# Optimization experiments

Measured on AMD Instinct MI355X. Metric: run time of the kernel, lower is better.

The kernel has to match this reference:

```python
import jax, jax.numpy as jnp
import numpy as np

NUM_HEADS = 16
GROUP_NUM = 4
HIDDEN = 1024
HEAD_DIM = HIDDEN // NUM_HEADS
EPS = 1e-5


def layernorm(x, g, b):
    mu = jnp.mean(x, axis=-1, keepdims=True)
    var = jnp.var(x, axis=-1, keepdims=True)
    return (x - mu) * jax.lax.rsqrt(var + EPS) * g + b


def setup_inputs() -> dict:
    key = jax.random.key(0)
    ks = jax.random.split(key, 12)
    s = 0.02
    return {
        "hidden_state": jax.random.normal(ks[0], (2, 2048, HIDDEN), jnp.float32),
        "wq": jax.random.normal(ks[1], (HIDDEN, HIDDEN), jnp.float32) * s,
        "bq": jnp.zeros((HIDDEN,), jnp.float32),
        "wk": jax.random.normal(ks[2], (GROUP_NUM * HEAD_DIM, HIDDEN), jnp.float32) * s,
        "bk": jnp.zeros((GROUP_NUM * HEAD_DIM,), jnp.float32),
        "wv": jax.random.normal(ks[3], (GROUP_NUM * HEAD_DIM, HIDDEN), jnp.float32) * s,
        "bv": jnp.zeros((GROUP_NUM * HEAD_DIM,), jnp.float32),
        "wo": jax.random.normal(ks[4], (HIDDEN, HIDDEN), jnp.float32) * s,
        "bo": jnp.zeros((HIDDEN,), jnp.float32),
        "ln_g": jnp.ones((HIDDEN,), jnp.float32),
        "ln_b": jnp.zeros((HIDDEN,), jnp.float32),
        "w1": jax.random.normal(ks[5], (HIDDEN, HIDDEN), jnp.float32) * s,
        "b1": jnp.zeros((HIDDEN,), jnp.float32),
        "w2": jax.random.normal(ks[6], (HIDDEN, HIDDEN), jnp.float32) * s,
        "b2": jnp.zeros((HIDDEN,), jnp.float32),
        "fln_g": jnp.ones((HIDDEN,), jnp.float32),
        "fln_b": jnp.zeros((HIDDEN,), jnp.float32),
    }


def reference(hidden_state, wq, bq, wk, bk, wv, bv, wo, bo, ln_g, ln_b,
              w1, b1, w2, b2, fln_g, fln_b):
    B, S, H = hidden_state.shape
    hpg = NUM_HEADS // GROUP_NUM  # heads per KV group

    q = hidden_state @ wq.T + bq  # [B,S,H]
    k = hidden_state @ wk.T + bk  # [B,S,G*D]
    v = hidden_state @ wv.T + bv

    q = q.reshape(B, S, NUM_HEADS, HEAD_DIM).transpose(0, 2, 1, 3)      # [B,Hh,S,D]
    k = k.reshape(B, S, GROUP_NUM, HEAD_DIM).transpose(0, 2, 1, 3)      # [B,G,S,D]
    v = v.reshape(B, S, GROUP_NUM, HEAD_DIM).transpose(0, 2, 1, 3)
    # expand KV groups to full head count (consecutive repeat, matching torch expand+reshape)
    k = jnp.repeat(k, hpg, axis=1)  # [B,Hh,S,D]
    v = jnp.repeat(v, hpg, axis=1)

    scale = 1.0 / jnp.sqrt(jnp.float32(HEAD_DIM))
    scores = jnp.einsum('bhsd,bhtd->bhst', q, k) * scale  # [B,Hh,S,S]
    probs = jax.nn.softmax(scores, axis=-1)
    attn = jnp.einsum('bhst,bhtd->bhsd', probs, v)  # [B,Hh,S,D]

    # Faithful to source: transpose(-1,-2) then raw flat view to [B, S, Hh*D]
    attn = jnp.swapaxes(attn, -1, -2).reshape(B, -1, HEAD_DIM * NUM_HEADS)

    out = layernorm(hidden_state + attn @ wo.T + bo, ln_g, ln_b)
    ffn = out @ w1.T + b1
    ffn = jax.nn.relu(ffn) @ w2.T + b2
    return layernorm(out + ffn, fln_g, fln_b)
```

## Files before the change

kernel.cpp:

```cpp
#include <hip/hip_runtime.h>
#include <math.h>

#define HIDDEN 1024
#define SEQ 2048

typedef __attribute__((ext_vector_type(8))) short short8;
typedef __attribute__((ext_vector_type(4))) float f32x4;

__device__ __forceinline__ unsigned short f2bf(float x) {
  union { float f; unsigned u; } c; c.f = x;
  unsigned r = c.u + 0x7FFFu + ((c.u >> 16) & 1u);
  return (unsigned short)(r >> 16);
}
__device__ __forceinline__ float bf2f(unsigned short h) {
  union { unsigned u; float f; } c; c.u = ((unsigned)h) << 16;
  return c.f;
}

__device__ __forceinline__ float fexp2(float x) {
  float r; asm("v_exp_f32 %0, %1" : "=v"(r) : "v"(x)); return r;
}

__device__ __forceinline__ unsigned cvt_pk_bf16(float lo, float hi) {
  unsigned r;
  asm("v_cvt_pk_bf16_f32 %0, %1, %2" : "=v"(r) : "v"(lo), "v"(hi));
  return r;
}

__device__ __forceinline__ void async_copy16(const void* g, void* l) {
  __builtin_amdgcn_global_load_lds(
      (const __attribute__((address_space(1))) unsigned int*)g,
      (__attribute__((address_space(3))) unsigned int*)l, 16, 0, 0);
}

__global__ __launch_bounds__(256) void cvt_all(
    const float* __restrict__ hs, const float* __restrict__ wq,
    const float* __restrict__ wk, const float* __restrict__ wv,
    const float* __restrict__ wo, const float* __restrict__ w1,
    const float* __restrict__ w2,
    unsigned short* __restrict__ hsb, unsigned short* __restrict__ wqb,
    unsigned short* __restrict__ wkb, unsigned short* __restrict__ wvb,
    unsigned short* __restrict__ wob, unsigned short* __restrict__ w1b,
    unsigned short* __restrict__ w2b)
{
  const int i = blockIdx.x * 256 + threadIdx.x;
  const float* src; unsigned short* dst; int off;
  if (i < 1048576)      { src = hs; dst = hsb; off = i; }
  else if (i < 1310720) { src = wq; dst = wqb; off = i - 1048576; }
  else if (i < 1376256) { src = wk; dst = wkb; off = i - 1310720; }
  else if (i < 1441792) { src = wv; dst = wvb; off = i - 1376256; }
  else if (i < 1703936) { src = wo; dst = wob; off = i - 1441792; }
  else if (i < 1966080) { src = w1; dst = w1b; off = i - 1703936; }
  else                  { src = w2; dst = w2b; off = i - 1966080; }
  float4 v = ((const float4*)src)[off];
  ushort4 o;
  o.x = f2bf(v.x); o.y = f2bf(v.y); o.z = f2bf(v.z); o.w = f2bf(v.w);
  ((ushort4*)dst)[off] = o;
}

template<bool RELU>
__global__ __launch_bounds__(256, 3) void gemm_wn(
    const unsigned short* __restrict__ A, const unsigned short* __restrict__ W,
    const float* __restrict__ bias, unsigned short* __restrict__ C,
    int M, int N, int K)
{
  __shared__ unsigned short As[2][64 * 64];
  __shared__ unsigned short Bs[2][128 * 64];

  const int flat = blockIdx.x;
  const int swz = (flat & 7) * ((int)gridDim.x >> 3) + (flat >> 3);
  const int ntx = N >> 7;
  const int m0 = (swz / ntx) * 64, n0 = (swz % ntx) * 128;

  const int tid = threadIdx.x;
  const int lane = tid & 63, wave = tid >> 6;
  const int ln = lane & 15, quad = lane >> 4;
  const int wm = (wave >> 1) * 32, wn = (wave & 1) * 64;

  f32x4 acc[2][4];
#pragma unroll
  for (int i = 0; i < 2; ++i)
#pragma unroll
    for (int j = 0; j < 4; ++j) acc[i][j] = (f32x4){0.f, 0.f, 0.f, 0.f};

  for (int k0 = 0; k0 < K; k0 += 128) {
#pragma unroll
    for (int half = 0; half < 2; ++half) {
      const int kh = k0 + half * 64;
#pragma unroll
      for (int it = 0; it < 2; ++it) {
        const int c = (wave * 2 + it) * 64 + lane;
        const int row = c >> 3, gc = (c & 7) ^ (row & 7);
        async_copy16(A + (size_t)(m0 + row) * K + kh + gc * 8,
                     &As[half][(wave * 2 + it) * 512]);
      }
#pragma unroll
      for (int it = 0; it < 4; ++it) {
        const int c = (wave * 4 + it) * 64 + lane;
        const int row = c >> 3, gc = (c & 7) ^ (row & 7);
        async_copy16(W + (size_t)(n0 + row) * K + kh + gc * 8,
                     &Bs[half][(wave * 4 + it) * 512]);
      }
    }
    __syncthreads();

#pragma unroll
    for (int half = 0; half < 2; ++half) {
      short8 af[2][2], bfr[4][2];
#pragma unroll
      for (int i = 0; i < 2; ++i) {
        const int row = wm + i * 16 + ln;
#pragma unroll
        for (int f = 0; f < 2; ++f) {
          const int ch = row * 8 + ((f * 4 + quad) ^ (row & 7));
          af[i][f] = *(const short8*)&As[half][ch * 8];
        }
      }
#pragma unroll
      for (int j = 0; j < 4; ++j) {
        const int row = wn + j * 16 + ln;
#pragma unroll
        for (int f = 0; f < 2; ++f) {
          const int ch = row * 8 + ((f * 4 + quad) ^ (row & 7));
          bfr[j][f] = *(const short8*)&Bs[half][ch * 8];
        }
      }
#pragma unroll
      for (int i = 0; i < 2; ++i)
#pragma unroll
        for (int j = 0; j < 4; ++j) {
          acc[i][j] = __builtin_amdgcn_mfma_f32_16x16x32_bf16(af[i][0], bfr[j][0], acc[i][j], 0, 0, 0);
          acc[i][j] = __builtin_amdgcn_mfma_f32_16x16x32_bf16(af[i][1], bfr[j][1], acc[i][j], 0, 0, 0);
        }
    }
    __syncthreads();
  }

#pragma unroll
  for (int j = 0; j < 4; ++j) {
    const int n = n0 + wn + j * 16 + ln;
    const float bv = bias[n];
#pragma unroll
    for (int i = 0; i < 2; ++i) {
#pragma unroll
      for (int rr = 0; rr < 4; ++rr) {
        const int m = m0 + wm + i * 16 + quad * 4 + rr;
        float v = acc[i][j][rr] + bv;
        if (RELU) v = fmaxf(v, 0.f);
        C[(size_t)m * N + n] = f2bf(v);
      }
    }
  }
}

__global__ __launch_bounds__(256) void gemm_qkv(
    const unsigned short* __restrict__ A,
    const unsigned short* __restrict__ Wq, const unsigned short* __restrict__ Wk,
    const unsigned short* __restrict__ Wv,
    const float* __restrict__ bq, const float* __restrict__ bk,
    const float* __restrict__ bv,
    unsigned short* __restrict__ Qo, unsigned short* __restrict__ Ko,
    unsigned short* __restrict__ Vt)
{
  __shared__ unsigned short As[64 * 64];
  __shared__ unsigned short Bs[128 * 64];

  const int flat = blockIdx.x;
  const int swz = (flat & 7) * 96 + (flat >> 3);
  const int bx = swz % 12, by = swz / 12;

  int mode, nw0;
  const unsigned short* W;
  const float* bias;
  if (bx < 8)       { mode = 0; W = Wq; bias = bq; nw0 = bx * 128; }
  else if (bx < 10) { mode = 1; W = Wk; bias = bk; nw0 = (bx - 8) * 128; }
  else              { mode = 2; W = Wv; bias = bv; nw0 = (bx - 10) * 128; }

  const int tid = threadIdx.x;
  const int lane = tid & 63, wave = tid >> 6;
  const int ln = lane & 15, quad = lane >> 4;
  const int wm = (wave >> 1) * 32, wn = (wave & 1) * 64;
  const int m0 = by * 64;
  const int K = 1024;

  f32x4 acc[2][4];
#pragma unroll
  for (int i = 0; i < 2; ++i)
#pragma unroll
    for (int j = 0; j < 4; ++j) acc[i][j] = (f32x4){0.f, 0.f, 0.f, 0.f};

  for (int k0 = 0; k0 < K; k0 += 64) {
#pragma unroll
    for (int it = 0; it < 2; ++it) {
      const int c = (wave * 2 + it) * 64 + lane;
      const int row = c >> 3, gc = (c & 7) ^ (row & 7);
      async_copy16(A + (size_t)(m0 + row) * K + k0 + gc * 8,
                   &As[(wave * 2 + it) * 512]);
    }
#pragma unroll
    for (int it = 0; it < 4; ++it) {
      const int c = (wave * 4 + it) * 64 + lane;
      const int row = c >> 3, gc = (c & 7) ^ (row & 7);
      async_copy16(W + (size_t)(nw0 + row) * K + k0 + gc * 8,
                   &Bs[(wave * 4 + it) * 512]);
    }
    __syncthreads();

    short8 af[2][2], bfr[4][2];
#pragma unroll
    for (int i = 0; i < 2; ++i) {
      const int row = wm + i * 16 + ln;
#pragma unroll
      for (int f = 0; f < 2; ++f) {
        const int ch = row * 8 + ((f * 4 + quad) ^ (row & 7));
        af[i][f] = *(const short8*)&As[ch * 8];
      }
    }
#pragma unroll
    for (int j = 0; j < 4; ++j) {
      const int row = wn + j * 16 + ln;
#pragma unroll
      for (int f = 0; f < 2; ++f) {
        const int ch = row * 8 + ((f * 4 + quad) ^ (row & 7));
        bfr[j][f] = *(const short8*)&Bs[ch * 8];
      }
    }
#pragma unroll
    for (int i = 0; i < 2; ++i)
#pragma unroll
      for (int j = 0; j < 4; ++j) {
        acc[i][j] = __builtin_amdgcn_mfma_f32_16x16x32_bf16(af[i][0], bfr[j][0], acc[i][j], 0, 0, 0);
        acc[i][j] = __builtin_amdgcn_mfma_f32_16x16x32_bf16(af[i][1], bfr[j][1], acc[i][j], 0, 0, 0);
      }
    __syncthreads();
  }

#pragma unroll
  for (int j = 0; j < 4; ++j) {
    const int nl = nw0 + wn + j * 16 + ln;
    const float bvv = bias[nl];
#pragma unroll
    for (int i = 0; i < 2; ++i) {
#pragma unroll
      for (int rr = 0; rr < 4; ++rr) {
        const int m = m0 + wm + i * 16 + quad * 4 + rr;
        const float v = acc[i][j][rr] + bvv;
        if (mode == 0) {
          Qo[(size_t)m * 1024 + nl] = f2bf(v);
        } else if (mode == 1) {
          Ko[(size_t)m * 256 + nl] = f2bf(v);
        } else {
          const int b = m >> 11, s = m & 2047;
          Vt[((size_t)b * 256 + nl) * SEQ + s] = f2bf(v);
        }
      }
    }
  }
}

__global__ __launch_bounds__(256, 2) void attn_mfma(
    const unsigned short* __restrict__ Q, const unsigned short* __restrict__ Kb,
    const unsigned short* __restrict__ Vt,
    unsigned short* __restrict__ N0, unsigned short* __restrict__ N1,
    float* __restrict__ LS)
{
  __shared__ unsigned short Ks[2][64 * 64];
  __shared__ unsigned short Vs[2][64 * 64];

  const int hwb = blockIdx.x;
  const int swz = (hwb & 7) * 64 + (hwb >> 3);
  const int qblk = swz & 7, half = (swz >> 3) & 1, h = (swz >> 4) & 15, b = swz >> 8;
  const int g = h >> 2;

  unsigned short* __restrict__ numO = half ? N1 : N0;
  float* __restrict__ lsO = LS + half * 65536;

  const int tid = threadIdx.x, lane = tid & 63, wave = tid >> 6;
  const int ln = lane & 15, quad = lane >> 4, q8 = quad * 8;
  const int s0 = qblk * 256;
  const float qscale = 0.125f * 1.44269504f;

  const int ln7 = ln & 7;
  const int x0 = (quad ^ ln7) * 8;
  const int x1 = ((4 + quad) ^ ln7) * 8;

  short8 ones;
#pragma unroll
  for (int e = 0; e < 8; ++e) ones[e] = (short)0x3F80;

  short8 qf[4][2];
#pragma unroll
  for (int qg = 0; qg < 4; ++qg) {
    const unsigned short* qsrc =
        Q + ((size_t)(b * SEQ + s0 + wave * 64 + qg * 16 + ln)) * 1024 + h * 64 + q8;
    qf[qg][0] = *(const short8*)qsrc;
    qf[qg][1] = *(const short8*)(qsrc + 32);
#pragma unroll
    for (int e = 0; e < 8; ++e) {
      qf[qg][0][e] = (short)f2bf(bf2f((unsigned short)qf[qg][0][e]) * qscale);
      qf[qg][1][e] = (short)f2bf(bf2f((unsigned short)qf[qg][1][e]) * qscale);
    }
  }

  const int srow = lane >> 3;
  const int sgcc = (lane & 7) ^ srow;

  auto stage = [&](int t0, int p) {
#pragma unroll
    for (int it = 0; it < 2; ++it) {
      const int row = wave * 16 + it * 8 + srow;
      const int skey = (row & 32) | ((row & 8) << 1) | ((row & 4) << 1) |
                       ((row & 16) >> 2) | (row & 3);
      async_copy16(Kb + (size_t)(b * SEQ + t0 + skey) * 256 + g * 64 + sgcc * 8,
                   &Ks[p][(wave * 2 + it) * 512]);
      async_copy16(Vt + (size_t)(b * 256 + g * 64 + row) * SEQ + t0 + sgcc * 8,
                   &Vs[p][(wave * 2 + it) * 512]);
    }
  };

  f32x4 of[4][4];
  f32x4 ls[4];
#pragma unroll
  for (int qg = 0; qg < 4; ++qg) {
    ls[qg] = (f32x4){0.f, 0.f, 0.f, 0.f};
#pragma unroll
    for (int jd = 0; jd < 4; ++jd) of[qg][jd] = (f32x4){0.f, 0.f, 0.f, 0.f};
  }

  const int tbase = half * 16;
  stage(tbase * 64, 0);

  for (int tt = 0; tt < 16; ++tt) {
    const int p = tt & 1;
    if (tt < 15) {
      stage((tbase + tt + 1) * 64, p ^ 1);
      asm volatile("s_waitcnt vmcnt(4)" ::: "memory");
    } else {
      asm volatile("s_waitcnt vmcnt(0)" ::: "memory");
    }
    __builtin_amdgcn_s_barrier();
    asm volatile("" ::: "memory");

    short8 pf[4][2];
#pragma unroll
    for (int hf = 0; hf < 2; ++hf) {
      f32x4 sc[2][4];
#pragma unroll
      for (int jn = 0; jn < 4; ++jn) {
        const int krow = (jn * 16 + ln) * 64;
        const short8 kf0 = *(const short8*)&Ks[p][krow + x0];
        const short8 kf1 = *(const short8*)&Ks[p][krow + x1];
#pragma unroll
        for (int q2 = 0; q2 < 2; ++q2) {
          const int qg = hf * 2 + q2;
          f32x4 z = (f32x4){0.f, 0.f, 0.f, 0.f};
          z = __builtin_amdgcn_mfma_f32_16x16x32_bf16(kf0, qf[qg][0], z, 0, 0, 0);
          z = __builtin_amdgcn_mfma_f32_16x16x32_bf16(kf1, qf[qg][1], z, 0, 0, 0);
          sc[q2][jn] = z;
        }
      }
#pragma unroll
      for (int q2 = 0; q2 < 2; ++q2) {
        const int qg = hf * 2 + q2;
#pragma unroll
        for (int jn = 0; jn < 4; ++jn)
#pragma unroll
          for (int r = 0; r < 4; ++r) sc[q2][jn][r] = fexp2(sc[q2][jn][r]);
#pragma unroll
        for (int F = 0; F < 2; ++F) {
          union { unsigned u[4]; short8 s; } pk;
          pk.u[0] = cvt_pk_bf16(sc[q2][2 * F][0], sc[q2][2 * F][1]);
          pk.u[1] = cvt_pk_bf16(sc[q2][2 * F][2], sc[q2][2 * F][3]);
          pk.u[2] = cvt_pk_bf16(sc[q2][2 * F + 1][0], sc[q2][2 * F + 1][1]);
          pk.u[3] = cvt_pk_bf16(sc[q2][2 * F + 1][2], sc[q2][2 * F + 1][3]);
          pf[qg][F] = pk.s;
        }
        ls[qg] = __builtin_amdgcn_mfma_f32_16x16x32_bf16(pf[qg][0], ones, ls[qg], 0, 0, 0);
        ls[qg] = __builtin_amdgcn_mfma_f32_16x16x32_bf16(pf[qg][1], ones, ls[qg], 0, 0, 0);
      }
    }

#pragma unroll
    for (int jd = 0; jd < 4; ++jd) {
      const int vrow = (jd * 16 + ln) * 64;
      const short8 vf0 = *(const short8*)&Vs[p][vrow + x0];
      const short8 vf1 = *(const short8*)&Vs[p][vrow + x1];
#pragma unroll
      for (int qg = 0; qg < 4; ++qg) {
        of[qg][jd] = __builtin_amdgcn_mfma_f32_16x16x32_bf16(pf[qg][0], vf0, of[qg][jd], 0, 0, 0);
        of[qg][jd] = __builtin_amdgcn_mfma_f32_16x16x32_bf16(pf[qg][1], vf1, of[qg][jd], 0, 0, 0);
      }
    }

    asm volatile("" ::: "memory");
    __builtin_amdgcn_s_barrier();
    asm volatile("" ::: "memory");
  }

#pragma unroll
  for (int qg = 0; qg < 4; ++qg) {
    const int sbase = s0 + wave * 64 + qg * 16 + quad * 4;
    if (ln == 0) {
#pragma unroll
      for (int r = 0; r < 4; ++r)
        lsO[(b * 16 + h) * 2048 + sbase + r] = ls[qg][r];
    }
#pragma unroll
    for (int jd = 0; jd < 4; ++jd) {
      const int d = jd * 16 + ln;
      ushort4 ov;
      ov.x = f2bf(of[qg][jd][0]);
      ov.y = f2bf(of[qg][jd][1]);
      ov.z = f2bf(of[qg][jd][2]);
      ov.w = f2bf(of[qg][jd][3]);
      *(ushort4*)&numO[((size_t)b * 1024 + h * 64 + d) * SEQ + sbase] = ov;
    }
  }
}

__global__ __launch_bounds__(256) void attn_reduce(
    const unsigned short* __restrict__ N0, unsigned short* att,
    const float* __restrict__ LS)
{
  const int i = (blockIdx.x * 256 + threadIdx.x) * 4;
  const int row = i >> 11, s = i & 2047;
  const int h = (row >> 6) & 15, b = row >> 10;
  const int lsi = (b * 16 + h) * 2048 + s;
  const float4 l0 = *(const float4*)&LS[lsi];
  const float4 l1 = *(const float4*)&LS[65536 + lsi];
  const ushort4 a = *(const ushort4*)&N0[i];
  const ushort4 c = *(const ushort4*)&att[i];
  ushort4 o;
  o.x = f2bf((bf2f(a.x) + bf2f(c.x)) / (l0.x + l1.x));
  o.y = f2bf((bf2f(a.y) + bf2f(c.y)) / (l0.y + l1.y));
  o.z = f2bf((bf2f(a.z) + bf2f(c.z)) / (l0.z + l1.z));
  o.w = f2bf((bf2f(a.w) + bf2f(c.w)) / (l0.w + l1.w));
  *(ushort4*)&att[i] = o;
}

__device__ __forceinline__ void ln_core(float x[4], const float* gam, const float* bet,
                                        int tid, float out[4]) {
  float s1 = x[0] + x[1] + x[2] + x[3];
  float s2 = x[0] * x[0] + x[1] * x[1] + x[2] * x[2] + x[3] * x[3];
#pragma unroll
  for (int off = 1; off < 64; off <<= 1) {
    s1 += __shfl_xor(s1, off);
    s2 += __shfl_xor(s2, off);
  }
  __shared__ float r1[4], r2[4];
  const int wave = tid >> 6;
  if ((tid & 63) == 0) { r1[wave] = s1; r2[wave] = s2; }
  __syncthreads();
  s1 = r1[0] + r1[1] + r1[2] + r1[3];
  s2 = r2[0] + r2[1] + r2[2] + r2[3];
  const float mu  = s1 * (1.0f / HIDDEN);
  const float var = s2 * (1.0f / HIDDEN) - mu * mu;
  const float inv = rsqrtf(var + 1e-5f);
  float4 gv = *(const float4*)&gam[tid * 4];
  float4 bv = *(const float4*)&bet[tid * 4];
  out[0] = (x[0] - mu) * inv * gv.x + bv.x;
  out[1] = (x[1] - mu) * inv * gv.y + bv.y;
  out[2] = (x[2] - mu) * inv * gv.z + bv.z;
  out[3] = (x[3] - mu) * inv * gv.w + bv.w;
}

__global__ __launch_bounds__(256) void resid_ln1(
    const float* __restrict__ X, const unsigned short* __restrict__ Y,
    const float* __restrict__ gam, const float* __restrict__ bet,
    unsigned short* __restrict__ outb)
{
  const int row = blockIdx.x, tid = threadIdx.x;
  const size_t base = (size_t)row * HIDDEN + tid * 4;
  float4 a = *(const float4*)&X[base];
  ushort4 yv = *(const ushort4*)&Y[base];
  float x[4] = {a.x + bf2f(yv.x), a.y + bf2f(yv.y), a.z + bf2f(yv.z), a.w + bf2f(yv.w)};
  float o[4];
  ln_core(x, gam, bet, tid, o);
  ushort4 ov;
  ov.x = f2bf(o[0]); ov.y = f2bf(o[1]); ov.z = f2bf(o[2]); ov.w = f2bf(o[3]);
  *(ushort4*)&outb[base] = ov;
}

__global__ __launch_bounds__(256) void resid_ln2(
    const unsigned short* __restrict__ X, const unsigned short* __restrict__ Y,
    const float* __restrict__ gam, const float* __restrict__ bet,
    float* __restrict__ out)
{
  const int row = blockIdx.x, tid = threadIdx.x;
  const size_t base = (size_t)row * HIDDEN + tid * 4;
  ushort4 xv = *(const ushort4*)&X[base];
  ushort4 yv = *(const ushort4*)&Y[base];
  float x[4] = {bf2f(xv.x) + bf2f(yv.x), bf2f(xv.y) + bf2f(yv.y),
                bf2f(xv.z) + bf2f(yv.z), bf2f(xv.w) + bf2f(yv.w)};
  float o[4];
  ln_core(x, gam, bet, tid, o);
  float4 ov; ov.x = o[0]; ov.y = o[1]; ov.z = o[2]; ov.w = o[3];
  *(float4*)&out[base] = ov;
}

extern "C" void kernel_launch(void* const* d_in, const int* in_sizes, int n_in,
                              void* d_out, int out_size, void* d_ws, size_t ws_size,
                              hipStream_t stream)
{
  (void)in_sizes; (void)n_in; (void)out_size; (void)ws_size;
  const float* hs  = (const float*)d_in[0];
  const float* wq  = (const float*)d_in[1];
  const float* bq  = (const float*)d_in[2];
  const float* wk  = (const float*)d_in[3];
  const float* bk  = (const float*)d_in[4];
  const float* wv  = (const float*)d_in[5];
  const float* bvp = (const float*)d_in[6];
  const float* wo  = (const float*)d_in[7];
  const float* bo  = (const float*)d_in[8];
  const float* lng = (const float*)d_in[9];
  const float* lnb = (const float*)d_in[10];
  const float* w1  = (const float*)d_in[11];
  const float* b1  = (const float*)d_in[12];
  const float* w2  = (const float*)d_in[13];
  const float* b2  = (const float*)d_in[14];
  const float* flg = (const float*)d_in[15];
  const float* flb = (const float*)d_in[16];
  float* out = (float*)d_out;

  unsigned short* w = (unsigned short*)d_ws;
  unsigned short* wqb = w;
  unsigned short* wkb = w + 1048576;
  unsigned short* wvb = w + 1310720;
  unsigned short* wob = w + 1572864;
  unsigned short* w1b = w + 2621440;
  unsigned short* w2b = w + 3670016;
  unsigned short* hsb = w + 4718592;
  unsigned short* qb  = w + 8912896;
  unsigned short* kb  = w + 13107200;
  unsigned short* vt  = w + 14155776;
  unsigned short* att = w + 15204352;
  unsigned short* f1b = hsb;
  unsigned short* yb  = qb;
  unsigned short* obb = att;
  unsigned short* f2b = qb;
  float* lsbuf = (float*)wqb;

  dim3 blk(256);
  cvt_all<<<dim3(8704), blk, 0, stream>>>(hs, wq, wk, wv, wo, w1, w2,
                                          hsb, wqb, wkb, wvb, wob, w1b, w2b);

  gemm_qkv<<<dim3(768), blk, 0, stream>>>(hsb, wqb, wkb, wvb, bq, bk, bvp,
                                          qb, kb, vt);
  attn_mfma<<<dim3(512), blk, 0, stream>>>(qb, kb, vt, hsb, att, lsbuf);
  attn_reduce<<<dim3(4096), blk, 0, stream>>>(hsb, att, lsbuf);
  gemm_wn<false><<<dim3(512), blk, 0, stream>>>(att, wob, bo, yb, 4096, 1024, 1024);
  resid_ln1<<<dim3(4096), blk, 0, stream>>>(hs, yb, lng, lnb, obb);
  gemm_wn<true><<<dim3(512), blk, 0, stream>>>(obb, w1b, b1, f1b, 4096, 1024, 1024);
  gemm_wn<false><<<dim3(512), blk, 0, stream>>>(f1b, w2b, b2, f2b, 4096, 1024, 1024);
  resid_ln2<<<dim3(4096), blk, 0, stream>>>(obb, f2b, flg, flb, out);
}
```

Baseline: 226.1 us.

## Use 128x128 GEMM tiles with double-buffered async prefetch for dense layers

The three 4096x1024x1024 GEMMs move from 64x128 tiles without overlap (load a 128-wide K chunk, sync, compute) to 128x128 tiles with a two-stage software pipeline. The next 64-wide K slice is prefetched while the current one is computed, using vmcnt waits and raw barriers. This increases operand reuse per block and hides global load latency. The cost is more accumulator registers and LDS per block and only 256 blocks, which is about one wave of blocks on the 256 CUs, so occupancy and tail balance may suffer.

```diff
diff --git a/kernel.cpp b/kernel.cpp
--- a/kernel.cpp
+++ b/kernel.cpp
@@ -59,81 +59,90 @@
 }
 
 template<bool RELU>
-__global__ __launch_bounds__(256, 3) void gemm_wn(
+__global__ __launch_bounds__(256) void gemm_big(
     const unsigned short* __restrict__ A, const unsigned short* __restrict__ W,
     const float* __restrict__ bias, unsigned short* __restrict__ C,
     int M, int N, int K)
 {
-  __shared__ unsigned short As[2][64 * 64];
+  __shared__ unsigned short As[2][128 * 64];
   __shared__ unsigned short Bs[2][128 * 64];
 
   const int flat = blockIdx.x;
   const int swz = (flat & 7) * ((int)gridDim.x >> 3) + (flat >> 3);
   const int ntx = N >> 7;
-  const int m0 = (swz / ntx) * 64, n0 = (swz % ntx) * 128;
+  const int m0 = (swz / ntx) * 128, n0 = (swz % ntx) * 128;
 
   const int tid = threadIdx.x;
   const int lane = tid & 63, wave = tid >> 6;
   const int ln = lane & 15, quad = lane >> 4;
-  const int wm = (wave >> 1) * 32, wn = (wave & 1) * 64;
-
-  f32x4 acc[2][4];
-#pragma unroll
-  for (int i = 0; i < 2; ++i)
+  const int wm = (wave >> 1) * 64, wn = (wave & 1) * 64;
+
+  f32x4 acc[4][4];
+#pragma unroll
+  for (int i = 0; i < 4; ++i)
 #pragma unroll
     for (int j = 0; j < 4; ++j) acc[i][j] = (f32x4){0.f, 0.f, 0.f, 0.f};
 
-  for (int k0 = 0; k0 < K; k0 += 128) {
-#pragma unroll
-    for (int half = 0; half < 2; ++half) {
-      const int kh = k0 + half * 64;
-#pragma unroll
-      for (int it = 0; it < 2; ++it) {
-        const int c = (wave * 2 + it) * 64 + lane;
-        const int row = c >> 3, gc = (c & 7) ^ (row & 7);
-        async_copy16(A + (size_t)(m0 + row) * K + kh + gc * 8,
-                     &As[half][(wave * 2 + it) * 512]);
-      }
-#pragma unroll
-      for (int it = 0; it < 4; ++it) {
-        const int c = (wave * 4 + it) * 64 + lane;
-        const int row = c >> 3, gc = (c & 7) ^ (row & 7);
-        async_copy16(W + (size_t)(n0 + row) * K + kh + gc * 8,
-                     &Bs[half][(wave * 4 + it) * 512]);
-      }
-    }
-    __syncthreads();
-
-#pragma unroll
-    for (int half = 0; half < 2; ++half) {
-      short8 af[2][2], bfr[4][2];
-#pragma unroll
-      for (int i = 0; i < 2; ++i) {
-        const int row = wm + i * 16 + ln;
-#pragma unroll
-        for (int f = 0; f < 2; ++f) {
-          const int ch = row * 8 + ((f * 4 + quad) ^ (row & 7));
-          af[i][f] = *(const short8*)&As[half][ch * 8];
-        }
-      }
+  auto stage = [&](int k0, int p) {
+#pragma unroll
+    for (int it = 0; it < 4; ++it) {
+      const int c = (wave * 4 + it) * 64 + lane;
+      const int row = c >> 3, gc = (c & 7) ^ (row & 7);
+      async_copy16(A + (size_t)(m0 + row) * K + k0 + gc * 8,
+                   &As[p][(wave * 4 + it) * 512]);
+    }
+#pragma unroll
+    for (int it = 0; it < 4; ++it) {
+      const int c = (wave * 4 + it) * 64 + lane;
+      const int row = c >> 3, gc = (c & 7) ^ (row & 7);
+      async_copy16(W + (size_t)(n0 + row) * K + k0 + gc * 8,
+                   &Bs[p][(wave * 4 + it) * 512]);
+    }
+  };
+
+  stage(0, 0);
+  const int NT = K >> 6;
+  for (int t = 0; t < NT; ++t) {
+    const int p = t & 1;
+    if (t < NT - 1) {
+      stage((t + 1) * 64, p ^ 1);
+      asm volatile("s_waitcnt vmcnt(8)" ::: "memory");
+    } else {
+      asm volatile("s_waitcnt vmcnt(0)" ::: "memory");
+    }
+    __builtin_amdgcn_s_barrier();
+    asm volatile("" ::: "memory");
+
+    short8 af[4][2], bfr[4][2];
+#pragma unroll
+    for (int i = 0; i < 4; ++i) {
+      const int row = wm + i * 16 + ln;
+#pragma unroll
+      for (int f = 0; f < 2; ++f) {
+        const int ch = row * 8 + ((f * 4 + quad) ^ (row & 7));
+        af[i][f] = *(const short8*)&As[p][ch * 8];
+      }
+    }
+#pragma unroll
+    for (int j = 0; j < 4; ++j) {
+      const int row = wn + j * 16 + ln;
+#pragma unroll
+      for (int f = 0; f < 2; ++f) {
+        const int ch = row * 8 + ((f * 4 + quad) ^ (row & 7));
+        bfr[j][f] = *(const short8*)&Bs[p][ch * 8];
+      }
+    }
+#pragma unroll
+    for (int i = 0; i < 4; ++i)
 #pragma unroll
       for (int j = 0; j < 4; ++j) {
-        const int row = wn + j * 16 + ln;
-#pragma unroll
-        for (int f = 0; f < 2; ++f) {
-          const int ch = row * 8 + ((f * 4 + quad) ^ (row & 7));
-          bfr[j][f] = *(const short8*)&Bs[half][ch * 8];
-        }
-      }
-#pragma unroll
-      for (int i = 0; i < 2; ++i)
-#pragma unroll
-        for (int j = 0; j < 4; ++j) {
-          acc[i][j] = __builtin_amdgcn_mfma_f32_16x16x32_bf16(af[i][0], bfr[j][0], acc[i][j], 0, 0, 0);
-          acc[i][j] = __builtin_amdgcn_mfma_f32_16x16x32_bf16(af[i][1], bfr[j][1], acc[i][j], 0, 0, 0);
-        }
-    }
-    __syncthreads();
+        acc[i][j] = __builtin_amdgcn_mfma_f32_16x16x32_bf16(af[i][0], bfr[j][0], acc[i][j], 0, 0, 0);
+        acc[i][j] = __builtin_amdgcn_mfma_f32_16x16x32_bf16(af[i][1], bfr[j][1], acc[i][j], 0, 0, 0);
+      }
+
+    asm volatile("" ::: "memory");
+    __builtin_amdgcn_s_barrier();
+    asm volatile("" ::: "memory");
   }
 
 #pragma unroll
@@ -141,7 +150,7 @@
     const int n = n0 + wn + j * 16 + ln;
     const float bv = bias[n];
 #pragma unroll
-    for (int i = 0; i < 2; ++i) {
+    for (int i = 0; i < 4; ++i) {
 #pragma unroll
       for (int rr = 0; rr < 4; ++rr) {
         const int m = m0 + wm + i * 16 + quad * 4 + rr;
@@ -548,9 +557,9 @@
                                           qb, kb, vt);
   attn_mfma<<<dim3(512), blk, 0, stream>>>(qb, kb, vt, hsb, att, lsbuf);
   attn_reduce<<<dim3(4096), blk, 0, stream>>>(hsb, att, lsbuf);
-  gemm_wn<false><<<dim3(512), blk, 0, stream>>>(att, wob, bo, yb, 4096, 1024, 1024);
+  gemm_big<false><<<dim3(256), blk, 0, stream>>>(att, wob, bo, yb, 4096, 1024, 1024);
   resid_ln1<<<dim3(4096), blk, 0, stream>>>(hs, yb, lng, lnb, obb);
-  gemm_wn<true><<<dim3(512), blk, 0, stream>>>(obb, w1b, b1, f1b, 4096, 1024, 1024);
-  gemm_wn<false><<<dim3(512), blk, 0, stream>>>(f1b, w2b, b2, f2b, 4096, 1024, 1024);
+  gemm_big<true><<<dim3(256), blk, 0, stream>>>(obb, w1b, b1, f1b, 4096, 1024, 1024);
+  gemm_big<false><<<dim3(256), blk, 0, stream>>>(f1b, w2b, b2, f2b, 4096, 1024, 1024);
   resid_ln2<<<dim3(4096), blk, 0, stream>>>(obb, f2b, flg, flb, out);
 }
```

Result: slower. 241.6 us (+6.8%).

## Split-K the output and FFN GEMMs into two partials combined downstream

Applied to the files above, without the earlier changes.

The three 4096x1024x1024 GEMMs become a split-K kernel that launches twice as many blocks, each covering half of K. Each half writes its own bf16 partial buffer, and the partials are summed with the bias in the residual-LayerNorm kernels or in a new combine+ReLU kernel. The goal is more blocks in flight and better occupancy, since the kernel now uses single-buffered 64-wide K steps with a smaller shared footprint. The cost is extra global traffic for the partial buffers, one additional elementwise launch, and lower precision from rounding each partial to bf16.

```diff
diff --git a/kernel.cpp b/kernel.cpp
--- a/kernel.cpp
+++ b/kernel.cpp
@@ -58,19 +58,23 @@
   ((ushort4*)dst)[off] = o;
 }
 
-template<bool RELU>
-__global__ __launch_bounds__(256, 3) void gemm_wn(
+__global__ __launch_bounds__(256) void gemm_sk(
     const unsigned short* __restrict__ A, const unsigned short* __restrict__ W,
-    const float* __restrict__ bias, unsigned short* __restrict__ C,
+    unsigned short* __restrict__ P0, unsigned short* __restrict__ P1,
     int M, int N, int K)
 {
-  __shared__ unsigned short As[2][64 * 64];
-  __shared__ unsigned short Bs[2][128 * 64];
+  __shared__ unsigned short As[64 * 64];
+  __shared__ unsigned short Bs[128 * 64];
 
   const int flat = blockIdx.x;
   const int swz = (flat & 7) * ((int)gridDim.x >> 3) + (flat >> 3);
+  const int halfn = (int)gridDim.x >> 1;
+  const int kh = swz >= halfn;
+  const int rem = swz & (halfn - 1);
   const int ntx = N >> 7;
-  const int m0 = (swz / ntx) * 64, n0 = (swz % ntx) * 128;
+  const int m0 = (rem / ntx) * 64, n0 = (rem % ntx) * 128;
+  const int kbase = kh * (K >> 1);
+  unsigned short* __restrict__ Pd = kh ? P1 : P0;
 
   const int tid = threadIdx.x;
   const int lane = tid & 63, wave = tid >> 6;
@@ -83,74 +87,82 @@
 #pragma unroll
     for (int j = 0; j < 4; ++j) acc[i][j] = (f32x4){0.f, 0.f, 0.f, 0.f};
 
-  for (int k0 = 0; k0 < K; k0 += 128) {
-#pragma unroll
-    for (int half = 0; half < 2; ++half) {
-      const int kh = k0 + half * 64;
-#pragma unroll
-      for (int it = 0; it < 2; ++it) {
-        const int c = (wave * 2 + it) * 64 + lane;
-        const int row = c >> 3, gc = (c & 7) ^ (row & 7);
-        async_copy16(A + (size_t)(m0 + row) * K + kh + gc * 8,
-                     &As[half][(wave * 2 + it) * 512]);
-      }
-#pragma unroll
-      for (int it = 0; it < 4; ++it) {
-        const int c = (wave * 4 + it) * 64 + lane;
-        const int row = c >> 3, gc = (c & 7) ^ (row & 7);
-        async_copy16(W + (size_t)(n0 + row) * K + kh + gc * 8,
-                     &Bs[half][(wave * 4 + it) * 512]);
-      }
+  const int kend = kbase + (K >> 1);
+  for (int k0 = kbase; k0 < kend; k0 += 64) {
+#pragma unroll
+    for (int it = 0; it < 2; ++it) {
+      const int c = (wave * 2 + it) * 64 + lane;
+      const int row = c >> 3, gc = (c & 7) ^ (row & 7);
+      async_copy16(A + (size_t)(m0 + row) * K + k0 + gc * 8,
+                   &As[(wave * 2 + it) * 512]);
+    }
+#pragma unroll
+    for (int it = 0; it < 4; ++it) {
+      const int c = (wave * 4 + it) * 64 + lane;
+      const int row = c >> 3, gc = (c & 7) ^ (row & 7);
+      async_copy16(W + (size_t)(n0 + row) * K + k0 + gc * 8,
+                   &Bs[(wave * 4 + it) * 512]);
     }
     __syncthreads();
 
-#pragma unroll
-    for (int half = 0; half < 2; ++half) {
-      short8 af[2][2], bfr[4][2];
-#pragma unroll
-      for (int i = 0; i < 2; ++i) {
-        const int row = wm + i * 16 + ln;
-#pragma unroll
-        for (int f = 0; f < 2; ++f) {
-          const int ch = row * 8 + ((f * 4 + quad) ^ (row & 7));
-          af[i][f] = *(const short8*)&As[half][ch * 8];
-        }
-      }
+    short8 af[2][2], bfr[4][2];
+#pragma unroll
+    for (int i = 0; i < 2; ++i) {
+      const int row = wm + i * 16 + ln;
+#pragma unroll
+      for (int f = 0; f < 2; ++f) {
+        const int ch = row * 8 + ((f * 4 + quad) ^ (row & 7));
+        af[i][f] = *(const short8*)&As[ch * 8];
+      }
+    }
+#pragma unroll
+    for (int j = 0; j < 4; ++j) {
+      const int row = wn + j * 16 + ln;
+#pragma unroll
+      for (int f = 0; f < 2; ++f) {
+        const int ch = row * 8 + ((f * 4 + quad) ^ (row & 7));
+        bfr[j][f] = *(const short8*)&Bs[ch * 8];
+      }
+    }
+#pragma unroll
+    for (int i = 0; i < 2; ++i)
 #pragma unroll
       for (int j = 0; j < 4; ++j) {
-        const int row = wn + j * 16 + ln;
-#pragma unroll
-        for (int f = 0; f < 2; ++f) {
-          const int ch = row * 8 + ((f * 4 + quad) ^ (row & 7));
-          bfr[j][f] = *(const short8*)&Bs[half][ch * 8];
-        }
-      }
-#pragma unroll
-      for (int i = 0; i < 2; ++i)
-#pragma unroll
-        for (int j = 0; j < 4; ++j) {
-          acc[i][j] = __builtin_amdgcn_mfma_f32_16x16x32_bf16(af[i][0], bfr[j][0], acc[i][j], 0, 0, 0);
-          acc[i][j] = __builtin_amdgcn_mfma_f32_16x16x32_bf16(af[i][1], bfr[j][1], acc[i][j], 0, 0, 0);
-        }
-    }
+        acc[i][j] = __builtin_amdgcn_mfma_f32_16x16x32_bf16(af[i][0], bfr[j][0], acc[i][j], 0, 0, 0);
+        acc[i][j] = __builtin_amdgcn_mfma_f32_16x16x32_bf16(af[i][1], bfr[j][1], acc[i][j], 0, 0, 0);
+      }
     __syncthreads();
   }
 
 #pragma unroll
   for (int j = 0; j < 4; ++j) {
     const int n = n0 + wn + j * 16 + ln;
-    const float bv = bias[n];
 #pragma unroll
     for (int i = 0; i < 2; ++i) {
 #pragma unroll
       for (int rr = 0; rr < 4; ++rr) {
         const int m = m0 + wm + i * 16 + quad * 4 + rr;
-        float v = acc[i][j][rr] + bv;
-        if (RELU) v = fmaxf(v, 0.f);
-        C[(size_t)m * N + n] = f2bf(v);
-      }
-    }
-  }
+        Pd[(size_t)m * N + n] = f2bf(acc[i][j][rr]);
+      }
+    }
+  }
+}
+
+__global__ __launch_bounds__(256) void comb_relu(
+    const unsigned short* __restrict__ P0, const unsigned short* __restrict__ P1,
+    const float* __restrict__ bias, unsigned short* __restrict__ out)
+{
+  const int i = (blockIdx.x * 256 + threadIdx.x) * 4;
+  const int col = i & 1023;
+  const ushort4 a = *(const ushort4*)&P0[i];
+  const ushort4 b = *(const ushort4*)&P1[i];
+  const float4 bv = *(const float4*)&bias[col];
+  ushort4 o;
+  o.x = f2bf(fmaxf(bf2f(a.x) + bf2f(b.x) + bv.x, 0.f));
+  o.y = f2bf(fmaxf(bf2f(a.y) + bf2f(b.y) + bv.y, 0.f));
+  o.z = f2bf(fmaxf(bf2f(a.z) + bf2f(b.z) + bv.z, 0.f));
+  o.w = f2bf(fmaxf(bf2f(a.w) + bf2f(b.w) + bv.w, 0.f));
+  *(ushort4*)&out[i] = o;
 }
 
 __global__ __launch_bounds__(256) void gemm_qkv(
@@ -465,15 +477,22 @@
 }
 
 __global__ __launch_bounds__(256) void resid_ln1(
-    const float* __restrict__ X, const unsigned short* __restrict__ Y,
+    const float* __restrict__ X,
+    const unsigned short* __restrict__ P0, const unsigned short* __restrict__ P1,
+    const float* __restrict__ bo,
     const float* __restrict__ gam, const float* __restrict__ bet,
     unsigned short* __restrict__ outb)
 {
   const int row = blockIdx.x, tid = threadIdx.x;
   const size_t base = (size_t)row * HIDDEN + tid * 4;
   float4 a = *(const float4*)&X[base];
-  ushort4 yv = *(const ushort4*)&Y[base];
-  float x[4] = {a.x + bf2f(yv.x), a.y + bf2f(yv.y), a.z + bf2f(yv.z), a.w + bf2f(yv.w)};
+  ushort4 p = *(const ushort4*)&P0[base];
+  ushort4 q = *(const ushort4*)&P1[base];
+  float4 bv = *(const float4*)&bo[tid * 4];
+  float x[4] = {a.x + bf2f(p.x) + bf2f(q.x) + bv.x,
+                a.y + bf2f(p.y) + bf2f(q.y) + bv.y,
+                a.z + bf2f(p.z) + bf2f(q.z) + bv.z,
+                a.w + bf2f(p.w) + bf2f(q.w) + bv.w};
   float o[4];
   ln_core(x, gam, bet, tid, o);
   ushort4 ov;
@@ -482,16 +501,22 @@
 }
 
 __global__ __launch_bounds__(256) void resid_ln2(
-    const unsigned short* __restrict__ X, const unsigned short* __restrict__ Y,
+    const unsigned short* __restrict__ X,
+    const unsigned short* __restrict__ P0, const unsigned short* __restrict__ P1,
+    const float* __restrict__ b2,
     const float* __restrict__ gam, const float* __restrict__ bet,
     float* __restrict__ out)
 {
   const int row = blockIdx.x, tid = threadIdx.x;
   const size_t base = (size_t)row * HIDDEN + tid * 4;
   ushort4 xv = *(const ushort4*)&X[base];
-  ushort4 yv = *(const ushort4*)&Y[base];
-  float x[4] = {bf2f(xv.x) + bf2f(yv.x), bf2f(xv.y) + bf2f(yv.y),
-                bf2f(xv.z) + bf2f(yv.z), bf2f(xv.w) + bf2f(yv.w)};
+  ushort4 p = *(const ushort4*)&P0[base];
+  ushort4 q = *(const ushort4*)&P1[base];
+  float4 bv = *(const float4*)&b2[tid * 4];
+  float x[4] = {bf2f(xv.x) + bf2f(p.x) + bf2f(q.x) + bv.x,
+                bf2f(xv.y) + bf2f(p.y) + bf2f(q.y) + bv.y,
+                bf2f(xv.z) + bf2f(p.z) + bf2f(q.z) + bv.z,
+                bf2f(xv.w) + bf2f(p.w) + bf2f(q.w) + bv.w};
   float o[4];
   ln_core(x, gam, bet, tid, o);
   float4 ov; ov.x = o[0]; ov.y = o[1]; ov.z = o[2]; ov.w = o[3];
@@ -534,10 +559,10 @@
   unsigned short* kb  = w + 13107200;
   unsigned short* vt  = w + 14155776;
   unsigned short* att = w + 15204352;
+  unsigned short* pa  = w + 19398656;
+  unsigned short* pb  = w + 23592960;
   unsigned short* f1b = hsb;
-  unsigned short* yb  = qb;
   unsigned short* obb = att;
-  unsigned short* f2b = qb;
   float* lsbuf = (float*)wqb;
 
   dim3 blk(256);
@@ -548,9 +573,13 @@
                                           qb, kb, vt);
   attn_mfma<<<dim3(512), blk, 0, stream>>>(qb, kb, vt, hsb, att, lsbuf);
   attn_reduce<<<dim3(4096), blk, 0, stream>>>(hsb, att, lsbuf);
-  gemm_wn<false><<<dim3(512), blk, 0, stream>>>(att, wob, bo, yb, 4096, 1024, 1024);
-  resid_ln1<<<dim3(4096), blk, 0, stream>>>(hs, yb, lng, lnb, obb);
-  gemm_wn<true><<<dim3(512), blk, 0, stream>>>(obb, w1b, b1, f1b, 4096, 1024, 1024);
-  gemm_wn<false><<<dim3(512), blk, 0, stream>>>(f1b, w2b, b2, f2b, 4096, 1024, 1024);
-  resid_ln2<<<dim3(4096), blk, 0, stream>>>(obb, f2b, flg, flb, out);
-}
+
+  gemm_sk<<<dim3(1024), blk, 0, stream>>>(att, wob, pa, pb, 4096, 1024, 1024);
+  resid_ln1<<<dim3(4096), blk, 0, stream>>>(hs, pa, pb, bo, lng, lnb, obb);
+
+  gemm_sk<<<dim3(1024), blk, 0, stream>>>(obb, w1b, pa, pb, 4096, 1024, 1024);
+  comb_relu<<<dim3(4096), blk, 0, stream>>>(pa, pb, b1, f1b);
+
+  gemm_sk<<<dim3(1024), blk, 0, stream>>>(f1b, w2b, pa, pb, 4096, 1024, 1024);
+  resid_ln2<<<dim3(4096), blk, 0, stream>>>(obb, pa, pb, b2, flg, flb, out);
+}
```

After: 244.5 us. +8.1%, slower.
